# Performance work log

Hardware: AMD Instinct MI355X
Metric: run time of the kernel (lower is better)

Reference implementation:

```python
import jax, jax.numpy as jnp
import numpy as np

# ---- static config (matches init_kwargs) ----
IMG = 56        # num_patches = image_size // patch_size = 112 // 2
WIN = 7         # window_size
SHIFT = 3       # shift_size
C = 256         # projection_dim
H = 8           # num_heads
DH = C // H     # head dim = 32
S = WIN * WIN   # tokens per window = 49
NY = IMG // WIN # windows per side = 8
NW = NY * NY    # windows per image = 64
NMLP = 1024
EPS = 1e-5
SCALE = DH ** (-0.5)


def _relative_position_index():
    ch, cw = np.meshgrid(np.arange(WIN), np.arange(WIN), indexing='ij')
    coords = np.stack([ch, cw]).reshape(2, -1)                 # [2, S]
    rel = coords[:, :, None] - coords[:, None, :]              # [2, S, S]
    rel = rel.transpose(1, 2, 0) + (WIN - 1)                   # [S, S, 2]
    idx = rel[:, :, 0] * (2 * WIN - 1) + rel[:, :, 1]          # [S, S]
    return idx.reshape(-1)                                     # [S*S]

REL_IDX = jnp.asarray(_relative_position_index(), dtype=jnp.int32)


def _attn_mask():
    # Faithful replication of the module's mask construction (incl. the empty
    h_slices = (slice(0, -WIN), slice(-WIN, -SHIFT), slice(-SHIFT, None))
    w_slices = (slice(0, -WIN), slice(-WIN, -WIN), slice(-SHIFT, None))
    m = np.zeros((IMG, IMG), dtype=np.float32)
    count = 0
    for hs in h_slices:
        for ws in w_slices:
            m[hs, ws] = count
            count += 1
    mw = m.reshape(NY, WIN, NY, WIN).transpose(0, 2, 1, 3).reshape(NW, S)
    diff = mw[:, None, :] - mw[:, :, None]
    return np.where(diff != 0, -100.0, 0.0).astype(np.float32)  # [NW, S, S]

ATTN_MASK = jnp.asarray(_attn_mask())


def _layernorm(x, gamma, beta):
    mu = jnp.mean(x, axis=-1, keepdims=True)
    var = jnp.mean(jnp.square(x - mu), axis=-1, keepdims=True)
    return (x - mu) * jax.lax.rsqrt(var + EPS) * gamma + beta


def setup_inputs() -> dict:
    key = jax.random.key(0)
    ks = jax.random.split(key, 12)
    B = 32
    s = lambda fan: 1.0 / np.sqrt(fan)
    return {
        'x': jax.random.normal(ks[0], (B, IMG * IMG, C), dtype=jnp.float32),
        'norm_gamma': jnp.ones((C,), jnp.float32),
        'norm_beta': jnp.zeros((C,), jnp.float32),
        'qkv_w': jax.random.normal(ks[1], (C, 3 * C), jnp.float32) * s(C),
        'qkv_b': jnp.zeros((3 * C,), jnp.float32),
        'proj_w': jax.random.normal(ks[2], (C, C), jnp.float32) * s(C),
        'proj_b': jnp.zeros((C,), jnp.float32),
        'rel_bias_table': jax.random.truncated_normal(ks[3], -2.0, 2.0, ((2 * WIN - 1) ** 2, H), jnp.float32) * 0.02,
        'mlp_w1': jax.random.normal(ks[4], (C, NMLP), jnp.float32) * s(C),
        'mlp_b1': jnp.zeros((NMLP,), jnp.float32),
        'mlp_w2': jax.random.normal(ks[5], (NMLP, C), jnp.float32) * s(NMLP),
        'mlp_b2': jnp.zeros((C,), jnp.float32),
    }


def reference(x, norm_gamma, norm_beta, qkv_w, qkv_b, proj_w, proj_b,
              rel_bias_table, mlp_w1, mlp_b1, mlp_w2, mlp_b2):
    B = x.shape[0]
    # ---- shifted-window attention block ----
    shortcut = x
    xn = _layernorm(x, norm_gamma, norm_beta).reshape(B, IMG, IMG, C)
    shifted = jnp.roll(xn, shift=(-SHIFT, -SHIFT), axis=(1, 2))
    # window partition -> [B*NW, S, C]
    xw = shifted.reshape(B, NY, WIN, NY, WIN, C).transpose(0, 1, 3, 2, 4, 5)
    xw = xw.reshape(B * NW, S, C)
    qkv = xw @ qkv_w + qkv_b                                    # [BnW, S, 3C]
    qkv = qkv.reshape(B * NW, S, 3, H, DH).transpose(2, 0, 3, 1, 4)
    q, k, v = qkv[0] * SCALE, qkv[1], qkv[2]                    # [BnW, H, S, DH]
    attn = jnp.einsum('whsd,whtd->whst', q, k)                  # [BnW, H, S, S]
    bias = rel_bias_table[REL_IDX].reshape(S, S, H).transpose(2, 0, 1)
    attn = attn + bias[None]
    attn = attn.reshape(B, NW, H, S, S) + ATTN_MASK[None, :, None]
    attn = jax.nn.softmax(attn.reshape(B * NW, H, S, S), axis=-1)
    out = jnp.einsum('whst,whtd->wshd', attn, v).reshape(B * NW, S, C)
    out = out @ proj_w + proj_b
    # window reverse + unshift
    out = out.reshape(B, NY, NY, WIN, WIN, C).transpose(0, 1, 3, 2, 4, 5)
    out = out.reshape(B, IMG, IMG, C)
    out = jnp.roll(out, shift=(SHIFT, SHIFT), axis=(1, 2)).reshape(B, IMG * IMG, C)
    x = shortcut + out
    # ---- MLP block (same LayerNorm weights reused, as in original) ----
    shortcut2 = x
    xn2 = _layernorm(x, norm_gamma, norm_beta)
    h = jax.nn.gelu(xn2 @ mlp_w1 + mlp_b1, approximate=False)
    h = h @ mlp_w2 + mlp_b2
    return shortcut2 + h
```

## Files before the change

kernel.cpp:

```cpp
#include <hip/hip_runtime.h>
#include <math.h>

#define IMG   56
#define WINSZ 7
#define SHIFTSZ 3
#define CDIM  256
#define NH    8
#define DH    32
#define SEQ   49
#define NYW   8
#define NWIN  64
#define NMLP  1024
#define BATCH 32
#define NTOK  (BATCH*IMG*IMG)
#define BNW   (BATCH*NWIN)
#define SZT   ((size_t)NTOK*CDIM)
#define QSCALE 0.17677669529663687f
#define EPSLN 1e-5f

typedef __attribute__((ext_vector_type(8))) short short8;
typedef __attribute__((ext_vector_type(4))) float f32x4;

__device__ __forceinline__ float bf2f(unsigned short u) {
    union { unsigned i; float f; } c; c.i = ((unsigned)u) << 16; return c.f;
}
__device__ __forceinline__ unsigned short f2bf(float f) {
    union { float f; unsigned i; } c; c.f = f;
    unsigned r = c.i + 0x7fffu + ((c.i >> 16) & 1u);
    return (unsigned short)(r >> 16);
}

__device__ __forceinline__ float gelu_f(float v) {
    float u = v * 0.70710678118654752f;
    float x = fabsf(u);
    float t = __builtin_amdgcn_rcpf(fmaf(0.3275911f, x, 1.0f));
    float e = __expf(-u * u);
    float p = fmaf(1.061405429f, t, -1.453152027f);
    p = fmaf(p, t, 1.421413741f);
    p = fmaf(p, t, -0.284496736f);
    p = fmaf(p, t, 0.254829592f);
    float er = 1.0f - p * t * e;
    er = copysignf(er, u);
    return 0.5f * v * (1.0f + er);
}

#define GLL16(gp, lp) __builtin_amdgcn_global_load_lds( \
    (__attribute__((address_space(1))) void*)(gp),      \
    (__attribute__((address_space(3))) void*)(lp), 16, 0, 0)

__global__ __launch_bounds__(256) void wtrans(const float* __restrict__ in,
                                              unsigned short* __restrict__ out,
                                              int K, int N) {
    int idx = blockIdx.x * 256 + threadIdx.x;
    if (idx >= K * N) return;
    int n = idx / K, k = idx - n * K;
    out[idx] = f2bf(in[(size_t)k * N + n]);
}

template<int WINDOWED>
__global__ __launch_bounds__(256) void ln_kernel(const float* __restrict__ x,
                                                 const float* __restrict__ gamma,
                                                 const float* __restrict__ beta,
                                                 unsigned short* __restrict__ out) {
    int wave = threadIdx.x >> 6;
    int lane = threadIdx.x & 63;
    int tok  = blockIdx.x * 4 + wave;
    int src  = tok;
    if (WINDOWED) {
        int b  = tok / (NWIN * SEQ);
        int r  = tok - b * (NWIN * SEQ);
        int wl = r / SEQ, s = r - wl * SEQ;
        int wy = wl >> 3, wx = wl & 7;
        int i  = s / WINSZ, j = s - i * WINSZ;
        int hp = wy * WINSZ + i + SHIFTSZ; if (hp >= IMG) hp -= IMG;
        int wp = wx * WINSZ + j + SHIFTSZ; if (wp >= IMG) wp -= IMG;
        src = b * (IMG * IMG) + hp * IMG + wp;
    }
    float4 v = *(const float4*)(x + (size_t)src * CDIM + lane * 4);
    float sum = v.x + v.y + v.z + v.w;
    float ss  = v.x*v.x + v.y*v.y + v.z*v.z + v.w*v.w;
#pragma unroll
    for (int off = 32; off; off >>= 1) {
        sum += __shfl_xor(sum, off);
        ss  += __shfl_xor(ss,  off);
    }
    float mu   = sum * (1.0f / CDIM);
    float var  = ss * (1.0f / CDIM) - mu * mu;
    float rstd = rsqrtf(var + EPSLN);
    float4 g  = *(const float4*)(gamma + lane * 4);
    float4 be = *(const float4*)(beta  + lane * 4);
    ushort4 o;
    o.x = f2bf((v.x - mu) * rstd * g.x + be.x);
    o.y = f2bf((v.y - mu) * rstd * g.y + be.y);
    o.z = f2bf((v.z - mu) * rstd * g.z + be.z);
    o.w = f2bf((v.w - mu) * rstd * g.w + be.w);
    *(ushort4*)(out + (size_t)tok * CDIM + lane * 4) = o;
}

#define EPI_QKV  0
#define EPI_PROJ 1
#define EPI_MLP1 2
#define EPI_MLP2 3

template<int EPI>
__global__ __launch_bounds__(256, 4)
void gemm_bt(const unsigned short* __restrict__ A,
             const unsigned short* __restrict__ Bt,
             int K,
             const float* __restrict__ bias,
             const float* __restrict__ resin,
             float* __restrict__ outF,
             unsigned short* __restrict__ outH) {
    __shared__ __align__(16) unsigned short As[2][128 * 32];
    __shared__ __align__(16) unsigned short Bs[2][128 * 32];
    int tid  = threadIdx.x;
    int lane = tid & 63, wave = tid >> 6;
    int q4   = lane >> 4, l16 = lane & 15;
    int wm   = wave >> 1, wn = wave & 1;

    int nwg = gridDim.x * gridDim.y;
    int f   = blockIdx.y * gridDim.x + blockIdx.x;
    int wg  = (f & 7) * (nwg >> 3) + (f >> 3);
    int by  = wg / gridDim.x;
    int bx  = wg - by * gridDim.x;
    int rowBase = by * 128;
    int colBase = bx * 128;

    f32x4 acc[4][4];
#pragma unroll
    for (int i = 0; i < 4; i++)
#pragma unroll
        for (int j = 0; j < 4; j++) acc[i][j] = (f32x4){0.f, 0.f, 0.f, 0.f};

    const unsigned short* Ab = A  + (size_t)rowBase * K;
    const unsigned short* Bb = Bt + (size_t)colBase * K;

    int r0 = wave * 32;
    int ra = r0 + (lane >> 2);
    int rb = ra + 16;
    int ca = (lane & 3) ^ ((ra >> 1) & 3);
    int cb = (lane & 3) ^ ((rb >> 1) & 3);
    const size_t off1 = (size_t)ra * K + ca * 8;
    const size_t off2 = (size_t)rb * K + cb * 8;

    auto stage = [&](int c, int k0) {
        GLL16(Ab + off1 + k0, &As[c][r0 * 32]);
        GLL16(Ab + off2 + k0, &As[c][(r0 + 16) * 32]);
        GLL16(Bb + off1 + k0, &Bs[c][r0 * 32]);
        GLL16(Bb + off2 + k0, &Bs[c][(r0 + 16) * 32]);
    };
    auto compute = [&](int c) {
        short8 af[4], bf[4];
#pragma unroll
        for (int mi = 0; mi < 4; mi++) {
            int r = wm * 64 + mi * 16 + l16;
            af[mi] = *(const short8*)&As[c][r * 32 + ((q4 ^ ((r >> 1) & 3)) * 8)];
        }
#pragma unroll
        for (int ni = 0; ni < 4; ni++) {
            int r = wn * 64 + ni * 16 + l16;
            bf[ni] = *(const short8*)&Bs[c][r * 32 + ((q4 ^ ((r >> 1) & 3)) * 8)];
        }
#pragma unroll
        for (int mi = 0; mi < 4; mi++)
#pragma unroll
            for (int ni = 0; ni < 4; ni++)
                acc[mi][ni] = __builtin_amdgcn_mfma_f32_16x16x32_bf16(
                    bf[ni], af[mi], acc[mi][ni], 0, 0, 0);
    };

    int nt = K >> 5;
    stage(0, 0);
    __syncthreads();
    int cur = 0;
    for (int t = 0; t < nt - 1; ++t) {
        stage(cur ^ 1, (t + 1) * 32);
        compute(cur);
        __syncthreads();
        cur ^= 1;
    }
    compute(cur);

    int mb = rowBase + wm * 64;
    int nb = colBase + wn * 64;
    float4 bias4[4];
#pragma unroll
    for (int ni = 0; ni < 4; ni++)
        bias4[ni] = *(const float4*)(bias + nb + ni * 16 + q4 * 4);

    if (EPI == EPI_QKV) {
        int three = colBase >> 8;
#pragma unroll
        for (int mi = 0; mi < 4; mi++) {
            int m = mb + mi * 16 + l16;
            int w = m / SEQ, s = m - w * SEQ;
#pragma unroll
            for (int ni = 0; ni < 4; ni++) {
                int n0 = nb + ni * 16 + q4 * 4;
                int hh = (n0 >> 5) & 7, dd0 = n0 & 31;
                const float* bp = (const float*)&bias4[ni];
                if (three == 2) {
#pragma unroll
                    for (int r = 0; r < 4; r++)
                        outH[2 * SZT + (((size_t)(w * NH + hh)) * DH + dd0 + r) * 64 + s] =
                            f2bf(acc[mi][ni][r] + bp[r]);
                } else {
                    float sc = (three == 0) ? QSCALE : 1.0f;
                    ushort4 o;
                    o.x = f2bf((acc[mi][ni][0] + bp[0]) * sc);
                    o.y = f2bf((acc[mi][ni][1] + bp[1]) * sc);
                    o.z = f2bf((acc[mi][ni][2] + bp[2]) * sc);
                    o.w = f2bf((acc[mi][ni][3] + bp[3]) * sc);
                    *(ushort4*)(outH + (size_t)three * SZT +
                                (((size_t)(w * NH + hh)) * SEQ + s) * DH + dd0) = o;
                }
            }
        }
    } else if (EPI == EPI_PROJ) {
#pragma unroll
        for (int mi = 0; mi < 4; mi++) {
            int m = mb + mi * 16 + l16;
            int w = m / SEQ, s = m - w * SEQ;
            int b = w >> 6, wl = w & 63;
            int wy = wl >> 3, wx = wl & 7;
            int ii = s / WINSZ, jj = s - ii * WINSZ;
            int hp = wy * WINSZ + ii + SHIFTSZ; if (hp >= IMG) hp -= IMG;
            int wp = wx * WINSZ + jj + SHIFTSZ; if (wp >= IMG) wp -= IMG;
            size_t tok = (size_t)b * (IMG * IMG) + hp * IMG + wp;
#pragma unroll
            for (int ni = 0; ni < 4; ni++) {
                int n0 = nb + ni * 16 + q4 * 4;
                float4 res = *(const float4*)(resin + tok * CDIM + n0);
                float4 o;
                o.x = acc[mi][ni][0] + bias4[ni].x + res.x;
                o.y = acc[mi][ni][1] + bias4[ni].y + res.y;
                o.z = acc[mi][ni][2] + bias4[ni].z + res.z;
                o.w = acc[mi][ni][3] + bias4[ni].w + res.w;
                *(float4*)(outF + tok * CDIM + n0) = o;
            }
        }
    } else if (EPI == EPI_MLP1) {
#pragma unroll
        for (int mi = 0; mi < 4; mi++) {
            int m = mb + mi * 16 + l16;
#pragma unroll
            for (int ni = 0; ni < 4; ni++) {
                int n0 = nb + ni * 16 + q4 * 4;
                ushort4 o;
                o.x = f2bf(gelu_f(acc[mi][ni][0] + bias4[ni].x));
                o.y = f2bf(gelu_f(acc[mi][ni][1] + bias4[ni].y));
                o.z = f2bf(gelu_f(acc[mi][ni][2] + bias4[ni].z));
                o.w = f2bf(gelu_f(acc[mi][ni][3] + bias4[ni].w));
                *(ushort4*)(outH + (size_t)m * NMLP + n0) = o;
            }
        }
    } else {
#pragma unroll
        for (int mi = 0; mi < 4; mi++) {
            int m = mb + mi * 16 + l16;
#pragma unroll
            for (int ni = 0; ni < 4; ni++) {
                int n0 = nb + ni * 16 + q4 * 4;
                float4 res = *(const float4*)(resin + (size_t)m * CDIM + n0);
                float4 o;
                o.x = acc[mi][ni][0] + bias4[ni].x + res.x;
                o.y = acc[mi][ni][1] + bias4[ni].y + res.y;
                o.z = acc[mi][ni][2] + bias4[ni].z + res.z;
                o.w = acc[mi][ni][3] + bias4[ni].w + res.w;
                *(float4*)(outF + (size_t)m * CDIM + n0) = o;
            }
        }
    }
}

__global__ __launch_bounds__(256) void attn_mfma(const unsigned short* __restrict__ qb,
                                                 const unsigned short* __restrict__ kb,
                                                 const unsigned short* __restrict__ vT,
                                                 const float* __restrict__ rel_tab,
                                                 unsigned short* __restrict__ outp) {
    __shared__ __align__(16) unsigned short Pl[4][64 * 64];
    __shared__ float tab[4][169];
    int tid  = threadIdx.x;
    int wave = tid >> 6, lane = tid & 63;
    int q4   = lane >> 4, l16 = lane & 15;
    int job  = blockIdx.x * 4 + wave;
    int w    = job >> 3, h = job & 7;

    for (int i = lane; i < 169; i += 64) tab[wave][i] = rel_tab[i * NH + h];

    const unsigned short* qg = qb + (size_t)(w * NH + h) * SEQ * DH;
    const unsigned short* kg = kb + (size_t)(w * NH + h) * SEQ * DH;
    short8 aq[4], bk[4];
#pragma unroll
    for (int mi = 0; mi < 4; mi++)
        aq[mi] = *(const short8*)(qg + (mi * 16 + l16) * DH + q4 * 8);
#pragma unroll
    for (int ni = 0; ni < 4; ni++)
        bk[ni] = *(const short8*)(kg + (ni * 16 + l16) * DH + q4 * 8);

    f32x4 acc[4][4];
#pragma unroll
    for (int i = 0; i < 4; i++)
#pragma unroll
        for (int j = 0; j < 4; j++) acc[i][j] = (f32x4){0.f, 0.f, 0.f, 0.f};
#pragma unroll
    for (int mi = 0; mi < 4; mi++)
#pragma unroll
        for (int ni = 0; ni < 4; ni++)
            acc[mi][ni] = __builtin_amdgcn_mfma_f32_16x16x32_bf16(
                aq[mi], bk[ni], acc[mi][ni], 0, 0, 0);

    int wl = w & 63;
    int wy = wl >> 3, wx = wl & 7;
    bool edge = (wy == 7) || (wx == 7);

    int itv[4], jtv[4], ltv[4];
#pragma unroll
    for (int ni = 0; ni < 4; ni++) {
        int t  = ni * 16 + l16;
        int it = (t * 37) >> 8;
        int jt = t - it * 7;
        itv[ni] = it; jtv[ni] = jt;
        int lab;
        if (wx == 7 && jt < 4) lab = 0;
        else {
            int lh = (wy == 7) ? ((it < 4) ? 1 : 2) : 0;
            lab = lh * 3 + ((wx == 7) ? 2 : 0);
        }
        ltv[ni] = lab;
    }

    float rinv[4][4];
#pragma unroll
    for (int mi = 0; mi < 4; mi++) {
#pragma unroll
        for (int r = 0; r < 4; r++) {
            int s  = mi * 16 + q4 * 4 + r;
            int is = (s * 37) >> 8;
            int js = s - is * 7;
            int lab_s;
            if (wx == 7 && js < 4) lab_s = 0;
            else {
                int lh = (wy == 7) ? ((is < 4) ? 1 : 2) : 0;
                lab_s = lh * 3 + ((wx == 7) ? 2 : 0);
            }
            float vv[4];
#pragma unroll
            for (int ni = 0; ni < 4; ni++) {
                int t = ni * 16 + l16;
                float a = acc[mi][ni][r];
                if (t < SEQ) {
                    int idx = (is - itv[ni] + 6) * 13 + (js - jtv[ni] + 6);
                    idx = idx < 0 ? 0 : (idx > 168 ? 168 : idx);
                    a += tab[wave][idx];
                    if (edge && lab_s != ltv[ni]) a -= 100.0f;
                } else {
                    a = -1e30f;
                }
                vv[ni] = a;
            }
            float mx = fmaxf(fmaxf(vv[0], vv[1]), fmaxf(vv[2], vv[3]));
#pragma unroll
            for (int off = 1; off < 16; off <<= 1) mx = fmaxf(mx, __shfl_xor(mx, off));
            float sm = 0.0f;
            unsigned short pb[4];
#pragma unroll
            for (int ni = 0; ni < 4; ni++) {
                float p = __expf(vv[ni] - mx);
                sm += p;
                pb[ni] = f2bf(p);
            }
#pragma unroll
            for (int off = 1; off < 16; off <<= 1) sm += __shfl_xor(sm, off);
            rinv[mi][r] = 1.0f / sm;
#pragma unroll
            for (int ni = 0; ni < 4; ni++) {
                int t  = ni * 16 + l16;
                int kbk = t >> 3, j = t & 7;
                Pl[wave][s * 64 + ((kbk ^ (s & 7)) * 8) + j] = pb[ni];
            }
        }
    }
    __syncthreads();

    short8 pa[4][2];
#pragma unroll
    for (int mi = 0; mi < 4; mi++)
#pragma unroll
        for (int ks = 0; ks < 2; ks++) {
            int m  = mi * 16 + l16;
            int kbk = ks * 4 + q4;
            pa[mi][ks] = *(const short8*)&Pl[wave][m * 64 + ((kbk ^ (m & 7)) * 8)];
        }
    const unsigned short* vg = vT + (size_t)(w * NH + h) * DH * 64;
    short8 bv[2][2];
#pragma unroll
    for (int n2 = 0; n2 < 2; n2++)
#pragma unroll
        for (int ks = 0; ks < 2; ks++)
            bv[n2][ks] = *(const short8*)(vg + (n2 * 16 + l16) * 64 + ks * 32 + q4 * 8);

    f32x4 o[4][2];
#pragma unroll
    for (int mi = 0; mi < 4; mi++)
#pragma unroll
        for (int n2 = 0; n2 < 2; n2++) o[mi][n2] = (f32x4){0.f, 0.f, 0.f, 0.f};
#pragma unroll
    for (int ks = 0; ks < 2; ks++)
#pragma unroll
        for (int mi = 0; mi < 4; mi++)
#pragma unroll
            for (int n2 = 0; n2 < 2; n2++)
                o[mi][n2] = __builtin_amdgcn_mfma_f32_16x16x32_bf16(
                    pa[mi][ks], bv[n2][ks], o[mi][n2], 0, 0, 0);

#pragma unroll
    for (int mi = 0; mi < 4; mi++)
#pragma unroll
        for (int r = 0; r < 4; r++) {
            int s = mi * 16 + q4 * 4 + r;
            if (s < SEQ) {
#pragma unroll
                for (int n2 = 0; n2 < 2; n2++) {
                    int d = n2 * 16 + l16;
                    outp[((size_t)w * SEQ + s) * CDIM + h * DH + d] =
                        f2bf(o[mi][n2][r] * rinv[mi][r]);
                }
            }
        }
}

extern "C" void kernel_launch(void* const* d_in, const int* in_sizes, int n_in,
                              void* d_out, int out_size, void* d_ws, size_t ws_size,
                              hipStream_t stream) {
    const float* x      = (const float*)d_in[0];
    const float* gamma  = (const float*)d_in[1];
    const float* beta   = (const float*)d_in[2];
    const float* qkv_w  = (const float*)d_in[3];
    const float* qkv_b  = (const float*)d_in[4];
    const float* proj_w = (const float*)d_in[5];
    const float* proj_b = (const float*)d_in[6];
    const float* rel_t  = (const float*)d_in[7];
    const float* mlp_w1 = (const float*)d_in[8];
    const float* mlp_b1 = (const float*)d_in[9];
    const float* mlp_w2 = (const float*)d_in[10];
    const float* mlp_b2 = (const float*)d_in[11];
    float* outp = (float*)d_out;

    const size_t VTSZ = (size_t)BNW * NH * DH * 64;
    unsigned short* xw_bf   = (unsigned short*)d_ws;
    unsigned short* qkv_bf  = xw_bf + SZT;
    unsigned short* attn_bf = qkv_bf + 2 * SZT + VTSZ;
    float*          y1      = (float*)(attn_bf + SZT);
    unsigned short* wt_bf   = (unsigned short*)(y1 + SZT);
    unsigned short* h_bf    = qkv_bf;

    unsigned short* qkvW  = wt_bf;
    unsigned short* projW = qkvW  + 768 * 256;
    unsigned short* mlp1W = projW + 256 * 256;
    unsigned short* mlp2W = mlp1W + 1024 * 256;

    wtrans<<<(768 * 256 + 255) / 256, 256, 0, stream>>>(qkv_w, qkvW, CDIM, 3 * CDIM);
    wtrans<<<(256 * 256 + 255) / 256, 256, 0, stream>>>(proj_w, projW, CDIM, CDIM);
    wtrans<<<(1024 * 256 + 255) / 256, 256, 0, stream>>>(mlp_w1, mlp1W, CDIM, NMLP);
    wtrans<<<(256 * 1024 + 255) / 256, 256, 0, stream>>>(mlp_w2, mlp2W, NMLP, CDIM);

    ln_kernel<1><<<NTOK / 4, 256, 0, stream>>>(x, gamma, beta, xw_bf);
    gemm_bt<EPI_QKV><<<dim3(6, NTOK / 128), 256, 0, stream>>>(
        xw_bf, qkvW, CDIM, qkv_b, nullptr, nullptr, qkv_bf);
    attn_mfma<<<BNW * NH / 4, 256, 0, stream>>>(
        qkv_bf, qkv_bf + SZT, qkv_bf + 2 * SZT, rel_t, attn_bf);
    gemm_bt<EPI_PROJ><<<dim3(2, NTOK / 128), 256, 0, stream>>>(
        attn_bf, projW, CDIM, proj_b, x, y1, nullptr);
    ln_kernel<0><<<NTOK / 4, 256, 0, stream>>>(y1, gamma, beta, xw_bf);
    gemm_bt<EPI_MLP1><<<dim3(8, NTOK / 128), 256, 0, stream>>>(
        xw_bf, mlp1W, CDIM, mlp_b1, nullptr, nullptr, h_bf);
    gemm_bt<EPI_MLP2><<<dim3(2, NTOK / 128), 256, 0, stream>>>(
        h_bf, mlp2W, NMLP, mlp_b2, y1, outp, nullptr);
}
```

Before: 694.6 us.

## Fuse projection GEMM with residual add and second LayerNorm

Replaces the projection GEMM plus separate LayerNorm kernel with one kernel whose 512-thread block covers a full 256-column row strip. Row sums and sums of squares are reduced across waves through shared memory, so the normalized bf16 MLP input is written directly from the epilogue. This avoids re-reading the fp32 residual output and one launch. In exchange, the blocks are larger and hold more registers and shared memory, and LayerNorm variance is computed in one pass as E[x^2]-mu^2.

```diff
diff --git a/kernel.cpp b/kernel.cpp
--- a/kernel.cpp
+++ b/kernel.cpp
@@ -98,7 +98,6 @@
 }
 
 #define EPI_QKV  0
-#define EPI_PROJ 1
 #define EPI_MLP1 2
 #define EPI_MLP2 3
 
@@ -216,29 +215,6 @@
                 }
             }
         }
-    } else if (EPI == EPI_PROJ) {
-#pragma unroll
-        for (int mi = 0; mi < 4; mi++) {
-            int m = mb + mi * 16 + l16;
-            int w = m / SEQ, s = m - w * SEQ;
-            int b = w >> 6, wl = w & 63;
-            int wy = wl >> 3, wx = wl & 7;
-            int ii = s / WINSZ, jj = s - ii * WINSZ;
-            int hp = wy * WINSZ + ii + SHIFTSZ; if (hp >= IMG) hp -= IMG;
-            int wp = wx * WINSZ + jj + SHIFTSZ; if (wp >= IMG) wp -= IMG;
-            size_t tok = (size_t)b * (IMG * IMG) + hp * IMG + wp;
-#pragma unroll
-            for (int ni = 0; ni < 4; ni++) {
-                int n0 = nb + ni * 16 + q4 * 4;
-                float4 res = *(const float4*)(resin + tok * CDIM + n0);
-                float4 o;
-                o.x = acc[mi][ni][0] + bias4[ni].x + res.x;
-                o.y = acc[mi][ni][1] + bias4[ni].y + res.y;
-                o.z = acc[mi][ni][2] + bias4[ni].z + res.z;
-                o.w = acc[mi][ni][3] + bias4[ni].w + res.w;
-                *(float4*)(outF + tok * CDIM + n0) = o;
-            }
-        }
     } else if (EPI == EPI_MLP1) {
 #pragma unroll
         for (int mi = 0; mi < 4; mi++) {
@@ -269,6 +245,158 @@
                 o.w = acc[mi][ni][3] + bias4[ni].w + res.w;
                 *(float4*)(outF + (size_t)m * CDIM + n0) = o;
             }
+        }
+    }
+}
+
+__global__ __launch_bounds__(512, 4)
+void gemm_proj_ln(const unsigned short* __restrict__ A,
+                  const unsigned short* __restrict__ Bt,
+                  const float* __restrict__ bias,
+                  const float* __restrict__ resin,
+                  const float* __restrict__ gamma,
+                  const float* __restrict__ beta,
+                  float* __restrict__ outY,
+                  unsigned short* __restrict__ outXW) {
+    const int K = CDIM;
+    __shared__ __align__(16) unsigned short As[2][128 * 32];
+    __shared__ __align__(16) unsigned short Bs[2][256 * 32];
+    __shared__ float2 redl[8][4][16];
+    int tid  = threadIdx.x;
+    int lane = tid & 63, wave = tid >> 6;
+    int q4   = lane >> 4, l16 = lane & 15;
+    int wm   = wave >> 2, wn = wave & 3;
+
+    int rowBase = blockIdx.x * 128;
+
+    f32x4 acc[4][4];
+#pragma unroll
+    for (int i = 0; i < 4; i++)
+#pragma unroll
+        for (int j = 0; j < 4; j++) acc[i][j] = (f32x4){0.f, 0.f, 0.f, 0.f};
+
+    const unsigned short* Ab = A + (size_t)rowBase * K;
+
+    int r0a = wave * 16;
+    int ra1 = r0a + (lane >> 2);
+    int r0b = wave * 32;
+    int rb1 = r0b + (lane >> 2);
+    int rb2 = rb1 + 16;
+    int ca1 = (lane & 3) ^ ((ra1 >> 1) & 3);
+    int cb1 = (lane & 3) ^ ((rb1 >> 1) & 3);
+    int cb2 = (lane & 3) ^ ((rb2 >> 1) & 3);
+    const size_t offA1 = (size_t)ra1 * K + ca1 * 8;
+    const size_t offB1 = (size_t)rb1 * K + cb1 * 8;
+    const size_t offB2 = (size_t)rb2 * K + cb2 * 8;
+
+    auto stage = [&](int c, int k0) {
+        GLL16(Ab + offA1 + k0, &As[c][r0a * 32]);
+        GLL16(Bt + offB1 + k0, &Bs[c][r0b * 32]);
+        GLL16(Bt + offB2 + k0, &Bs[c][(r0b + 16) * 32]);
+    };
+    auto compute = [&](int c) {
+        short8 af[4], bf[4];
+#pragma unroll
+        for (int mi = 0; mi < 4; mi++) {
+            int r = wm * 64 + mi * 16 + l16;
+            af[mi] = *(const short8*)&As[c][r * 32 + ((q4 ^ ((r >> 1) & 3)) * 8)];
+        }
+#pragma unroll
+        for (int ni = 0; ni < 4; ni++) {
+            int r = wn * 64 + ni * 16 + l16;
+            bf[ni] = *(const short8*)&Bs[c][r * 32 + ((q4 ^ ((r >> 1) & 3)) * 8)];
+        }
+#pragma unroll
+        for (int mi = 0; mi < 4; mi++)
+#pragma unroll
+            for (int ni = 0; ni < 4; ni++)
+                acc[mi][ni] = __builtin_amdgcn_mfma_f32_16x16x32_bf16(
+                    bf[ni], af[mi], acc[mi][ni], 0, 0, 0);
+    };
+
+    int nt = K >> 5;
+    stage(0, 0);
+    __syncthreads();
+    int cur = 0;
+    for (int t = 0; t < nt - 1; ++t) {
+        stage(cur ^ 1, (t + 1) * 32);
+        compute(cur);
+        __syncthreads();
+        cur ^= 1;
+    }
+    compute(cur);
+
+    int mb = rowBase + wm * 64;
+    int nb = wn * 64;
+    float4 bias4[4];
+#pragma unroll
+    for (int ni = 0; ni < 4; ni++)
+        bias4[ni] = *(const float4*)(bias + nb + ni * 16 + q4 * 4);
+
+    size_t tokv[4];
+    float s1[4], s2[4];
+#pragma unroll
+    for (int mi = 0; mi < 4; mi++) {
+        int m = mb + mi * 16 + l16;
+        int w = m / SEQ, s = m - w * SEQ;
+        int b = w >> 6, wl = w & 63;
+        int wy = wl >> 3, wx = wl & 7;
+        int ii = s / WINSZ, jj = s - ii * WINSZ;
+        int hp = wy * WINSZ + ii + SHIFTSZ; if (hp >= IMG) hp -= IMG;
+        int wp = wx * WINSZ + jj + SHIFTSZ; if (wp >= IMG) wp -= IMG;
+        size_t tok = (size_t)b * (IMG * IMG) + hp * IMG + wp;
+        tokv[mi] = tok;
+        float a = 0.f, q = 0.f;
+#pragma unroll
+        for (int ni = 0; ni < 4; ni++) {
+            int n0 = nb + ni * 16 + q4 * 4;
+            float4 res = *(const float4*)(resin + tok * CDIM + n0);
+            f32x4 y;
+            y[0] = acc[mi][ni][0] + bias4[ni].x + res.x;
+            y[1] = acc[mi][ni][1] + bias4[ni].y + res.y;
+            y[2] = acc[mi][ni][2] + bias4[ni].z + res.z;
+            y[3] = acc[mi][ni][3] + bias4[ni].w + res.w;
+            acc[mi][ni] = y;
+            *(float4*)(outY + tok * CDIM + n0) = *(float4*)&y;
+#pragma unroll
+            for (int r = 0; r < 4; r++) { a += y[r]; q += y[r] * y[r]; }
+        }
+        s1[mi] = a; s2[mi] = q;
+    }
+#pragma unroll
+    for (int mi = 0; mi < 4; mi++) {
+        s1[mi] += __shfl_xor(s1[mi], 16); s2[mi] += __shfl_xor(s2[mi], 16);
+        s1[mi] += __shfl_xor(s1[mi], 32); s2[mi] += __shfl_xor(s2[mi], 32);
+    }
+    if (q4 == 0) {
+#pragma unroll
+        for (int mi = 0; mi < 4; mi++)
+            redl[wave][mi][l16] = make_float2(s1[mi], s2[mi]);
+    }
+    __syncthreads();
+#pragma unroll
+    for (int mi = 0; mi < 4; mi++) {
+        float ts = 0.f, tq = 0.f;
+#pragma unroll
+        for (int w2 = 0; w2 < 4; w2++) {
+            float2 e = redl[wm * 4 + w2][mi][l16];
+            ts += e.x; tq += e.y;
+        }
+        float mu   = ts * (1.0f / CDIM);
+        float var  = tq * (1.0f / CDIM) - mu * mu;
+        float rstd = rsqrtf(var + EPSLN);
+        size_t tok = tokv[mi];
+#pragma unroll
+        for (int ni = 0; ni < 4; ni++) {
+            int n0 = nb + ni * 16 + q4 * 4;
+            float4 g  = *(const float4*)(gamma + n0);
+            float4 be = *(const float4*)(beta  + n0);
+            ushort4 o;
+            o.x = f2bf((acc[mi][ni][0] - mu) * rstd * g.x + be.x);
+            o.y = f2bf((acc[mi][ni][1] - mu) * rstd * g.y + be.y);
+            o.z = f2bf((acc[mi][ni][2] - mu) * rstd * g.z + be.z);
+            o.w = f2bf((acc[mi][ni][3] - mu) * rstd * g.w + be.w);
+            *(ushort4*)(outXW + tok * CDIM + n0) = o;
         }
     }
 }
@@ -470,9 +598,8 @@
         xw_bf, qkvW, CDIM, qkv_b, nullptr, nullptr, qkv_bf);
     attn_mfma<<<BNW * NH / 4, 256, 0, stream>>>(
         qkv_bf, qkv_bf + SZT, qkv_bf + 2 * SZT, rel_t, attn_bf);
-    gemm_bt<EPI_PROJ><<<dim3(2, NTOK / 128), 256, 0, stream>>>(
-        attn_bf, projW, CDIM, proj_b, x, y1, nullptr);
-    ln_kernel<0><<<NTOK / 4, 256, 0, stream>>>(y1, gamma, beta, xw_bf);
+    gemm_proj_ln<<<NTOK / 128, 512, 0, stream>>>(
+        attn_bf, projW, proj_b, x, gamma, beta, y1, xw_bf);
     gemm_bt<EPI_MLP1><<<dim3(8, NTOK / 128), 256, 0, stream>>>(
         xw_bf, mlp1W, CDIM, mlp_b1, nullptr, nullptr, h_bf);
     gemm_bt<EPI_MLP2><<<dim3(2, NTOK / 128), 256, 0, stream>>>(
```

Measured after the change: 692.7 us. No clear change (-0.3%).
